# Kernel tuning notes

Hardware: AMD Instinct MI355X
Metric: run time of the kernel (lower is better)

Reference implementation:

```python
import jax, jax.numpy as jnp
import numpy as np

H = 16  # num_heads


def setup_inputs() -> dict:
    key = jax.random.key(0)
    ks = jax.random.split(key, 8)
    B, S, d, L = 1, 2048, 1024, 8
    hd = d // H
    s = 0.02
    return {
        "x": jax.random.normal(ks[0], (B, S, d), jnp.float32),
        "past_values": jax.random.normal(ks[1], (L, B, H, S, hd), jnp.float32),
        "Wqkv": jax.random.normal(ks[2], (3 * d, d), jnp.float32) * s,
        "bqkv": jax.random.normal(ks[3], (3 * d,), jnp.float32) * s,
        "Wcol": jax.random.normal(ks[4], (d, d), jnp.float32) * s,
        "bcol": jax.random.normal(ks[5], (d,), jnp.float32) * s,
        "Wout": jax.random.normal(ks[6], (d, d), jnp.float32) * s,
        "bout": jax.random.normal(ks[7], (d,), jnp.float32) * s,
    }


def reference(x, past_values, Wqkv, bqkv, Wcol, bcol, Wout, bout):
    B, S, d = x.shape
    L = past_values.shape[0]
    hd = d // H
    scale = 1.0 / np.sqrt(hd).astype(np.float32)

    qkv = x @ Wqkv.T + bqkv                       # [B,S,3d]
    q, k, v = jnp.split(qkv, 3, axis=-1)

    def heads(t):                                  # [B,S,d] -> [B,H,S,hd]
        return t.reshape(B, S, H, hd).transpose(0, 2, 1, 3)

    q_row, k, v = heads(q), heads(k), heads(v)
    q_col = heads(x @ Wcol.T + bcol)

    # causal token scores [B,H,S,S]
    token_scores = jnp.einsum('bhqd,bhkd->bhqk', q_row, k) * scale
    causal = jnp.triu(jnp.ones((S, S), bool), 1)
    token_scores = jnp.where(causal, -jnp.inf, token_scores)

    # stack past values: torch stack(dim=3) -> [B,H,S,L,hd]; permute -> [B,S,L,H*hd]
    pv = past_values.transpose(1, 3, 0, 2, 4).reshape(B, S, L, d)
    ri = pv.reshape(B, S * L, d)
    mu = ri.mean(-1, keepdims=True)
    var = ri.var(-1, keepdims=True)
    ri = (ri - mu) / jnp.sqrt(var + 1e-5)          # F.layer_norm, no affine

    Wk, bk = Wqkv[d:2 * d], bqkv[d:2 * d]
    Wv, bv = Wqkv[2 * d:], bqkv[2 * d:]
    rk = (ri @ Wk.T + bk).reshape(B, S * L, H, hd).transpose(0, 2, 1, 3).reshape(B, H, S, L, hd)
    rv = (ri @ Wv.T + bv).reshape(B, S * L, H, hd).transpose(0, 2, 1, 3).reshape(B, H, S, L, hd)

    mem_scores = jnp.einsum('bhsd,bhsld->bhsl', q_col, rk) * scale  # [B,H,S,L]

    scores = jnp.concatenate([token_scores, mem_scores], axis=-1)   # [B,H,S,S+L]
    w = jax.nn.softmax(scores, axis=-1)
    tw, mw = w[..., :S], w[..., S:]

    ctx = jnp.einsum('bhqk,bhkd->bhqd', tw, v) + jnp.einsum('bhsl,bhsld->bhsd', mw, rv)
    out = ctx.transpose(0, 2, 1, 3).reshape(B, S, d)
    return out @ Wout.T + bout
```

## Files before the change

kernel.cpp:

```cpp
#include <hip/hip_runtime.h>
#include <math.h>

#define D   1024
#define H   16
#define HD  64
#define SEQ 2048
#define LL  8
#define SCALE 0.125f

typedef __attribute__((ext_vector_type(8))) __bf16 bf16x8;
typedef __attribute__((ext_vector_type(4))) float floatx4;
typedef __attribute__((ext_vector_type(8))) unsigned short ushort8;

__device__ inline unsigned short f32_to_bf16(float f) {
    unsigned int u = __builtin_bit_cast(unsigned int, f);
    u += 0x7FFF + ((u >> 16) & 1);
    return (unsigned short)(u >> 16);
}
__device__ inline float bf2f(unsigned short u) {
    unsigned int x = (unsigned int)u << 16;
    return __builtin_bit_cast(float, x);
}
__device__ inline void load_lds16(const void* g, void* l) {
    __builtin_amdgcn_global_load_lds(
        (__attribute__((address_space(1))) void*)g,
        (__attribute__((address_space(3))) void*)l, 16, 0, 0);
}

__device__ inline void xcd_swizzle(int& bx, int& by) {
    const int gx   = gridDim.x;
    const int lin  = blockIdx.y * gx + blockIdx.x;
    const int nblk = gx * gridDim.y;
    const int virt = (lin & 7) * (nblk >> 3) + (lin >> 3);
    bx = virt % gx;
    by = virt / gx;
}

#define NQ_X    524288
#define NQ_WQKV 786432
#define NQ_WC   262144
#define NQ_WO   262144
#define LN_BLK  16384
#define CVT_BLK 7168
#define PREP_GRID (LN_BLK + CVT_BLK + 4)

__global__ __launch_bounds__(256) void prep_kernel(
    const float* __restrict__ pv, const float* __restrict__ x,
    const float* __restrict__ Wqkv, const float* __restrict__ Wcol,
    const float* __restrict__ Wout, const float* __restrict__ bqkv,
    const float* __restrict__ bcol,
    unsigned short* __restrict__ ri, unsigned short* __restrict__ xb,
    unsigned short* __restrict__ W4b, unsigned short* __restrict__ Woutb,
    float* __restrict__ b4)
{
    const int b = blockIdx.x;
    const int t = threadIdx.x;
    if (b < LN_BLK) {
        const int r = b;
        const int s = r >> 3, l = r & 7;
        const int h = t >> 4, e = (t & 15) * 4;
        const size_t src = (size_t)l * (H * SEQ * HD) + (size_t)h * (SEQ * HD)
                         + (size_t)s * HD + e;
        float4 v = *(const float4*)(pv + src);
        float sum = v.x + v.y + v.z + v.w;
        float sq  = v.x * v.x + v.y * v.y + v.z * v.z + v.w * v.w;
#pragma unroll
        for (int off = 32; off; off >>= 1) {
            sum += __shfl_xor(sum, off);
            sq  += __shfl_xor(sq, off);
        }
        __shared__ float red[8];
        if ((t & 63) == 0) { red[(t >> 6) * 2] = sum; red[(t >> 6) * 2 + 1] = sq; }
        __syncthreads();
        sum = red[0] + red[2] + red[4] + red[6];
        sq  = red[1] + red[3] + red[5] + red[7];
        const float mean = sum * (1.f / 1024.f);
        const float var  = sq * (1.f / 1024.f) - mean * mean;
        const float rstd = rsqrtf(var + 1e-5f);
        ushort4 o;
        o.x = f32_to_bf16((v.x - mean) * rstd);
        o.y = f32_to_bf16((v.y - mean) * rstd);
        o.z = f32_to_bf16((v.z - mean) * rstd);
        o.w = f32_to_bf16((v.w - mean) * rstd);
        *(ushort4*)(ri + (size_t)r * D + t * 4) = o;
    } else if (b < LN_BLK + CVT_BLK) {
        const int i = (b - LN_BLK) * 256 + t;
        const float* src; unsigned short* dst; int off;
        if (i < NQ_X)                        { src = x;    dst = xb;    off = i; }
        else if (i < NQ_X + NQ_WQKV)         { src = Wqkv; dst = W4b;   off = i - NQ_X; }
        else if (i < NQ_X + NQ_WQKV + NQ_WC) {
            float4 v = ((const float4*)Wcol)[i - NQ_X - NQ_WQKV];
            ushort4 o;
            o.x = f32_to_bf16(v.x); o.y = f32_to_bf16(v.y);
            o.z = f32_to_bf16(v.z); o.w = f32_to_bf16(v.w);
            ((ushort4*)(W4b))[NQ_WQKV + (i - NQ_X - NQ_WQKV)] = o;
            return;
        }
        else                                 { src = Wout; dst = Woutb; off = i - NQ_X - NQ_WQKV - NQ_WC; }
        float4 v = ((const float4*)src)[off];
        ushort4 o;
        o.x = f32_to_bf16(v.x); o.y = f32_to_bf16(v.y);
        o.z = f32_to_bf16(v.z); o.w = f32_to_bf16(v.w);
        ((ushort4*)dst)[off] = o;
    } else {
        const int q = (b - LN_BLK - CVT_BLK) * 256 + t;
        float4 v = (q < 768) ? ((const float4*)bqkv)[q] : ((const float4*)bcol)[q - 768];
        ((float4*)b4)[q] = v;
    }
}

__global__ __launch_bounds__(256) void wkt_kernel(
    const float* __restrict__ Wqkv, unsigned short* __restrict__ WkT)
{
    const int h = blockIdx.x >> 4, ct = blockIdx.x & 15;
    const int c0 = ct * 64;
    const int t = threadIdx.x;
    __shared__ float tile[64][68];
    {
        const int e  = t >> 2;
        const int c4 = (t & 3) * 16;
        const float* src = Wqkv + (size_t)(D + h * HD + e) * D + c0 + c4;
#pragma unroll
        for (int j = 0; j < 4; j++) {
            float4 v = ((const float4*)src)[j];
            *(float4*)&tile[e][c4 + j * 4] = v;
        }
    }
    __syncthreads();
    {
        const int c  = t >> 2;
        const int e0 = (t & 3) * 16;
        ushort8 o0, o1;
#pragma unroll
        for (int j = 0; j < 8; j++) o0[j] = f32_to_bf16(tile[e0 + j][c]);
#pragma unroll
        for (int j = 0; j < 8; j++) o1[j] = f32_to_bf16(tile[e0 + 8 + j][c]);
        unsigned short* dst = WkT + (size_t)h * (D * HD) + (size_t)(c0 + c) * HD + e0;
        *(ushort8*)dst       = o0;
        *(ushort8*)(dst + 8) = o1;
    }
}

__global__ __launch_bounds__(256) void vtr_kernel(
    const unsigned short* __restrict__ qkv4, unsigned short* __restrict__ VT)
{
    const int h = blockIdx.x & 15, kt = blockIdx.x >> 4;
    const int t = threadIdx.x;
    __shared__ unsigned short Vt[64][264];
    const int pr = t & 31, eg = t >> 5;
#pragma unroll
    for (int sub = 0; sub < 4; sub++) {
        const int j0 = kt * 256 + sub * 64;
        const unsigned short* v0 = qkv4 + (size_t)(j0 + 2 * pr) * 4096 + 2 * D + h * HD + eg * 8;
        ushort8 va = *(const ushort8*)v0;
        ushort8 vb = *(const ushort8*)(v0 + 4096);
#pragma unroll
        for (int j = 0; j < 8; j++) {
            unsigned int pk = (unsigned int)va[j] | ((unsigned int)vb[j] << 16);
            *(unsigned int*)&Vt[eg * 8 + j][sub * 64 + 2 * pr] = pk;
        }
    }
    __syncthreads();
#pragma unroll
    for (int it = 0; it < 8; it++) {
        const int idx = it * 256 + t;
        const int e = idx >> 5, ch = idx & 31;
        ushort8 v = *(const ushort8*)&Vt[e][ch * 8];
        *(ushort8*)(VT + (size_t)h * (HD * SEQ) + (size_t)e * SEQ + kt * 256 + ch * 8) = v;
    }
}

template <typename CT, bool HAS_BIAS>
__global__ __launch_bounds__(256) void gemm_bf16_kernel(
    const unsigned short* __restrict__ A, const unsigned short* __restrict__ W,
    const float* __restrict__ bias, CT* __restrict__ C,
    int K, int N, int lda, int ldw, int ldc,
    size_t zsA, size_t zsW, size_t zsC)
{
    A += (size_t)blockIdx.z * zsA;
    W += (size_t)blockIdx.z * zsW;
    C += (size_t)blockIdx.z * zsC;

    __shared__ unsigned short As[128 * 32];
    __shared__ unsigned short Ws[128 * 32];
    const int t    = threadIdx.x;
    const int wave = t >> 6, lane = t & 63;
    const int wm   = wave >> 1, wn = wave & 1;
    int bx, by;
    xcd_swizzle(bx, by);
    const int m0 = by * 128, n0 = bx * 128;

    floatx4 acc[4][4];
#pragma unroll
    for (int i = 0; i < 4; i++)
#pragma unroll
        for (int j = 0; j < 4; j++) acc[i][j] = (floatx4)0.f;

    const int lrow = lane >> 2;
    const int lcol = (lane & 3) * 8;
    const unsigned short* Ag = A + (size_t)(m0 + wave * 32 + lrow) * lda + lcol;
    const unsigned short* Wg = W + (size_t)(n0 + wave * 32 + lrow) * ldw + lcol;
    unsigned short* Asw = &As[wave * 32 * 32];
    unsigned short* Wsw = &Ws[wave * 32 * 32];
    const size_t rowskipA = (size_t)16 * lda;
    const size_t rowskipW = (size_t)16 * ldw;

    const int arow  = lane & 15;
    const int aquad = (lane >> 4) * 8;

    for (int k0 = 0; k0 < K; k0 += 32) {
        load_lds16(Ag + k0,             Asw);
        load_lds16(Ag + k0 + rowskipA,  Asw + 16 * 32);
        load_lds16(Wg + k0,             Wsw);
        load_lds16(Wg + k0 + rowskipW,  Wsw + 16 * 32);
        __syncthreads();

        bf16x8 af[4], wf[4];
#pragma unroll
        for (int mi = 0; mi < 4; mi++)
            af[mi] = *(const bf16x8*)&As[(wm * 64 + mi * 16 + arow) * 32 + aquad];
#pragma unroll
        for (int ni = 0; ni < 4; ni++)
            wf[ni] = *(const bf16x8*)&Ws[(wn * 64 + ni * 16 + arow) * 32 + aquad];
#pragma unroll
        for (int mi = 0; mi < 4; mi++)
#pragma unroll
            for (int ni = 0; ni < 4; ni++)
                acc[mi][ni] = __builtin_amdgcn_mfma_f32_16x16x32_bf16(
                    af[mi], wf[ni], acc[mi][ni], 0, 0, 0);
        __syncthreads();
    }

    const int crow = (lane >> 4) * 4, ccol = lane & 15;
#pragma unroll
    for (int mi = 0; mi < 4; mi++) {
#pragma unroll
        for (int ni = 0; ni < 4; ni++) {
            const int gm = m0 + wm * 64 + mi * 16 + crow;
            const int gn = n0 + wn * 64 + ni * 16 + ccol;
            float bb = 0.f;
            if constexpr (HAS_BIAS) bb = bias[gn];
#pragma unroll
            for (int r = 0; r < 4; r++) {
                float v = acc[mi][ni][r] + bb;
                if constexpr (sizeof(CT) == 2)
                    C[(size_t)(gm + r) * ldc + gn] = (CT)f32_to_bf16(v);
                else
                    C[(size_t)(gm + r) * ldc + gn] = v;
            }
        }
    }
}

#define US_STRIDE 1032

__global__ __launch_bounds__(256) void memsc_kernel(
    const unsigned short* __restrict__ U, const unsigned short* __restrict__ ri,
    const unsigned short* __restrict__ qkv4, const float* __restrict__ bqkv,
    float* __restrict__ scores)
{
    const int s = blockIdx.x;
    const int t = threadIdx.x;
    const int w = t >> 6, lane = t & 63;
    const int lrow = lane & 15;
    const int lkq  = (lane >> 4) * 8;

    __shared__ unsigned short Us[16 * US_STRIDE];
    __shared__ union {
        unsigned short riS[8 * US_STRIDE];
        float red[4][16][16];
    } R;
    __shared__ float qbS[H];

    {
        const unsigned short* src = U + (size_t)s * (H * D);
#pragma unroll
        for (int j = 0; j < 8; j++) {
            const int c = j * 256 + t;
            const int row = c >> 7, col = (c & 127) * 8;
            *(ushort8*)&Us[row * US_STRIDE + col] =
                *(const ushort8*)(src + row * D + col);
        }
    }
    {
        const unsigned short* src = ri + (size_t)s * (LL * D);
#pragma unroll
        for (int j = 0; j < 4; j++) {
            const int c = j * 256 + t;
            const int row = c >> 7, col = (c & 127) * 8;
            *(ushort8*)&R.riS[row * US_STRIDE + col] =
                *(const ushort8*)(src + row * D + col);
        }
    }
    {
        const int h = t >> 4, sub = t & 15;
        const unsigned short* qc = qkv4 + (size_t)s * 4096 + 3 * D + h * HD + sub * 4;
        const float* bk = bqkv + D + h * HD + sub * 4;
        float acc = 0.f;
#pragma unroll
        for (int j = 0; j < 4; j++) acc += bf2f(qc[j]) * bk[j];
#pragma unroll
        for (int off = 1; off < 16; off <<= 1) acc += __shfl_xor(acc, off);
        if (sub == 0) qbS[h] = acc;
    }
    __syncthreads();

    floatx4 acc = (floatx4)0.f;
    const int kbase = w * 256;
#pragma unroll
    for (int step = 0; step < 8; step++) {
        const int k0 = kbase + step * 32;
        bf16x8 af = *(const bf16x8*)&Us[lrow * US_STRIDE + k0 + lkq];
        bf16x8 bf = {};
        if (lrow < 8) bf = *(const bf16x8*)&R.riS[lrow * US_STRIDE + k0 + lkq];
        acc = __builtin_amdgcn_mfma_f32_16x16x32_bf16(af, bf, acc, 0, 0, 0);
    }
    __syncthreads();

    {
        const int crow = (lane >> 4) * 4, ccol = lane & 15;
#pragma unroll
        for (int r = 0; r < 4; r++) R.red[w][crow + r][ccol] = acc[r];
    }
    __syncthreads();

    if (t < H * LL) {
        const int h = t >> 3, l = t & 7;
        float v = R.red[0][h][l] + R.red[1][h][l] + R.red[2][h][l] + R.red[3][h][l];
        scores[((size_t)s * H + h) * LL + l] = (v + qbS[h]) * SCALE;
    }
}

__global__ __launch_bounds__(256, 3) void attn_split_kernel(
    const unsigned short* __restrict__ qkv4, const unsigned short* __restrict__ VT,
    float* __restrict__ Opart, float2* __restrict__ mlpart)
{
    const int t    = threadIdx.x;
    const int w    = t >> 6, lane = t & 63;
    const int lrow = lane & 15;
    const int lk   = (lane >> 4) * 8;
    const int rrow = (lane >> 4) * 4;
    const int lin  = blockIdx.x;
    const int hsp  = lin & 63, g = lin >> 6;
    const int s    = hsp >> 4, h = hsp & 15;
    const int qt   = 31 - g;
    const int q0   = qt * 64;
    const int n    = qt + 1;
    const int lo   = (s * n) >> 2, hi = ((s + 1) * n) >> 2;
    const int part = (h * 32 + qt) * 4 + s;

    __shared__ unsigned short Ks[2][64 * 72];
    __shared__ unsigned short Vs[2][64 * 72];
    __shared__ unsigned short Pb[4][16 * 72];
    unsigned short* Pw = Pb[w];

    bf16x8 qreg[2];
#pragma unroll
    for (int kst = 0; kst < 2; kst++) {
        ushort8 qu = *(const ushort8*)(qkv4 + (size_t)(q0 + w * 16 + lrow) * 4096
                                       + h * HD + kst * 32 + lk);
        ushort8 qs;
#pragma unroll
        for (int j = 0; j < 8; j++) qs[j] = f32_to_bf16(bf2f(qu[j]) * SCALE);
        qreg[kst] = __builtin_bit_cast(bf16x8, qs);
    }

    const int srow = t >> 3;
    const int scol = (t & 7) * 8;
    const unsigned short* Kg = qkv4 + D + h * HD;
    const unsigned short* Vg = VT + (size_t)h * (HD * SEQ);

    bf16x8 kr0, kr1, vr0, vr1;
    float m_i[4], l_i[4];
    floatx4 Oacc[4];
#pragma unroll
    for (int r = 0; r < 4; r++) { m_i[r] = -1e30f; l_i[r] = 0.f; }
#pragma unroll
    for (int et = 0; et < 4; et++) Oacc[et] = (floatx4)0.f;

    if (lo < hi) {
        const int j0 = lo * 64;
        kr0 = *(const bf16x8*)(Kg + (size_t)(j0 + srow) * 4096 + scol);
        kr1 = *(const bf16x8*)(Kg + (size_t)(j0 + 32 + srow) * 4096 + scol);
        vr0 = *(const bf16x8*)(Vg + (size_t)srow * SEQ + j0 + scol);
        vr1 = *(const bf16x8*)(Vg + (size_t)(srow + 32) * SEQ + j0 + scol);
    }

    int cur = 0;
    for (int jt = lo; jt < hi; jt++) {
        const int j0 = jt * 64;
        *(bf16x8*)&Ks[cur][srow * 72 + scol]        = kr0;
        *(bf16x8*)&Ks[cur][(srow + 32) * 72 + scol] = kr1;
        *(bf16x8*)&Vs[cur][srow * 72 + scol]        = vr0;
        *(bf16x8*)&Vs[cur][(srow + 32) * 72 + scol] = vr1;
        if (jt + 1 < hi) {
            const int j0n = (jt + 1) * 64;
            kr0 = *(const bf16x8*)(Kg + (size_t)(j0n + srow) * 4096 + scol);
            kr1 = *(const bf16x8*)(Kg + (size_t)(j0n + 32 + srow) * 4096 + scol);
            vr0 = *(const bf16x8*)(Vg + (size_t)srow * SEQ + j0n + scol);
            vr1 = *(const bf16x8*)(Vg + (size_t)(srow + 32) * SEQ + j0n + scol);
        }
        __syncthreads();

        floatx4 S[4];
#pragma unroll
        for (int nt = 0; nt < 4; nt++) S[nt] = (floatx4)0.f;
        __builtin_amdgcn_s_setprio(1);
#pragma unroll
        for (int kst = 0; kst < 2; kst++) {
#pragma unroll
            for (int nt = 0; nt < 4; nt++) {
                bf16x8 bk = *(const bf16x8*)&Ks[cur][(nt * 16 + lrow) * 72 + kst * 32 + lk];
                S[nt] = __builtin_amdgcn_mfma_f32_16x16x32_bf16(qreg[kst], bk, S[nt], 0, 0, 0);
            }
        }
        __builtin_amdgcn_s_setprio(0);

        if (jt != qt) {
#pragma unroll
            for (int r = 0; r < 4; r++) {
                float sc[4];
#pragma unroll
                for (int nt = 0; nt < 4; nt++) sc[nt] = S[nt][r];
                float mx = fmaxf(fmaxf(sc[0], sc[1]), fmaxf(sc[2], sc[3]));
#pragma unroll
                for (int off = 1; off < 16; off <<= 1)
                    mx = fmaxf(mx, __shfl_xor(mx, off));
                const bool keep = __all(mx <= m_i[r] + 8.f);
                const float newm = keep ? m_i[r] : fmaxf(m_i[r], mx);
                float ps = 0.f;
#pragma unroll
                for (int nt = 0; nt < 4; nt++) {
                    float pe = __expf(sc[nt] - newm);
                    ps += pe;
                    Pw[(rrow + r) * 72 + nt * 16 + lrow] = f32_to_bf16(pe);
                }
#pragma unroll
                for (int off = 1; off < 16; off <<= 1)
                    ps += __shfl_xor(ps, off);
                if (keep) {
                    l_i[r] += ps;
                } else {
                    const float alpha = __expf(m_i[r] - newm);
                    m_i[r] = newm;
                    l_i[r] = l_i[r] * alpha + ps;
#pragma unroll
                    for (int et = 0; et < 4; et++) Oacc[et][r] *= alpha;
                }
            }
        } else {
#pragma unroll
            for (int r = 0; r < 4; r++) {
                const int qg = q0 + w * 16 + rrow + r;
                float sc[4];
                float mx = -1e30f;
#pragma unroll
                for (int nt = 0; nt < 4; nt++) {
                    sc[nt] = S[nt][r];
                    if (j0 + nt * 16 + lrow > qg) sc[nt] = -1e30f;
                    mx = fmaxf(mx, sc[nt]);
                }
#pragma unroll
                for (int off = 1; off < 16; off <<= 1)
                    mx = fmaxf(mx, __shfl_xor(mx, off));
                const float newm  = fmaxf(m_i[r], mx);
                const float alpha = __expf(m_i[r] - newm);
                m_i[r] = newm;
                float ps = 0.f;
#pragma unroll
                for (int nt = 0; nt < 4; nt++) {
                    float pe = __expf(sc[nt] - newm);
                    ps += pe;
                    Pw[(rrow + r) * 72 + nt * 16 + lrow] = f32_to_bf16(pe);
                }
#pragma unroll
                for (int off = 1; off < 16; off <<= 1)
                    ps += __shfl_xor(ps, off);
                l_i[r] = l_i[r] * alpha + ps;
#pragma unroll
                for (int et = 0; et < 4; et++) Oacc[et][r] *= alpha;
            }
        }

        __builtin_amdgcn_s_setprio(1);
#pragma unroll
        for (int kst = 0; kst < 2; kst++) {
            bf16x8 ap = *(const bf16x8*)&Pw[lrow * 72 + kst * 32 + lk];
#pragma unroll
            for (int et = 0; et < 4; et++) {
                bf16x8 bv = *(const bf16x8*)&Vs[cur][(et * 16 + lrow) * 72 + kst * 32 + lk];
                Oacc[et] = __builtin_amdgcn_mfma_f32_16x16x32_bf16(ap, bv, Oacc[et], 0, 0, 0);
            }
        }
        __builtin_amdgcn_s_setprio(0);
        cur ^= 1;
    }

#pragma unroll
    for (int r = 0; r < 4; r++) {
        const int ql = w * 16 + rrow + r;
        if (lrow == 0) mlpart[(size_t)part * 64 + ql] = make_float2(m_i[r], l_i[r]);
#pragma unroll
        for (int et = 0; et < 4; et++)
            Opart[((size_t)part * 64 + ql) * 64 + et * 16 + lrow] = Oacc[et][r];
    }
}

__global__ __launch_bounds__(256) void attn_merge_kernel(
    const float* __restrict__ Opart, const float2* __restrict__ mlpart,
    const float* __restrict__ scores,
    float* __restrict__ tok, float* __restrict__ mwf, float* __restrict__ Pmem)
{
    const int blk = blockIdx.x;
    const int h = blk >> 5, qt = blk & 31;
    const int q0 = qt * 64;
    const int t = threadIdx.x, tx = t & 15, ty = t >> 4;
    const size_t pb = (size_t)blk * 4;
#pragma unroll
    for (int i = 0; i < 4; i++) {
        const int qi = ty * 4 + i, qg = q0 + qi;
        float2 ml[4];
#pragma unroll
        for (int ps = 0; ps < 4; ps++) ml[ps] = mlpart[(pb + ps) * 64 + qi];
        const float* msp = scores + ((size_t)qg * H + h) * LL;
        float ms[LL];
#pragma unroll
        for (int l = 0; l < LL; l++) ms[l] = msp[l];
        float M = ml[0].x;
#pragma unroll
        for (int ps = 1; ps < 4; ps++) M = fmaxf(M, ml[ps].x);
#pragma unroll
        for (int l = 0; l < LL; l++) M = fmaxf(M, ms[l]);
        float f[4], L = 0.f;
#pragma unroll
        for (int ps = 0; ps < 4; ps++) { f[ps] = __expf(ml[ps].x - M); L += ml[ps].y * f[ps]; }
        float pm[LL];
#pragma unroll
        for (int l = 0; l < LL; l++) { pm[l] = __expf(ms[l] - M); L += pm[l]; }
        const float rl = 1.f / L;
        float4 o = make_float4(0.f, 0.f, 0.f, 0.f);
#pragma unroll
        for (int ps = 0; ps < 4; ps++) {
            const float fs = f[ps] * rl;
            float4 op = *(const float4*)&Opart[((pb + ps) * 64 + qi) * 64 + tx * 4];
            o.x += op.x * fs; o.y += op.y * fs; o.z += op.z * fs; o.w += op.w * fs;
        }
        *(float4*)&tok[(size_t)qg * D + h * HD + tx * 4] = o;
        if (tx == 0) {
            float* mw = mwf + ((size_t)qg * H + h) * LL;
            float psum = 0.f;
#pragma unroll
            for (int l = 0; l < LL; l++) { float v = pm[l] * rl; mw[l] = v; psum += v; }
            Pmem[(size_t)qg * H + h] = psum;
        }
    }
}

__global__ __launch_bounds__(256) void rbar_kernel(
    const float* __restrict__ mwf, const unsigned short* __restrict__ ri,
    unsigned short* __restrict__ rbar)
{
    const int s = blockIdx.x, t = threadIdx.x;
    __shared__ unsigned short riS[LL * D];
    __shared__ float wS[H * LL];
    {
        const unsigned short* src = ri + (size_t)s * (LL * D);
#pragma unroll
        for (int j = 0; j < 4; j++) {
            const int off = (j * 256 + t) * 8;
            *(ushort8*)&riS[off] = *(const ushort8*)(src + off);
        }
    }
    if (t < H * LL) wS[t] = mwf[(size_t)s * (H * LL) + t];
    __syncthreads();
    const int c4 = t * 4;
#pragma unroll
    for (int hh = 0; hh < H; hh++) {
        float v0 = 0.f, v1 = 0.f, v2 = 0.f, v3 = 0.f;
#pragma unroll
        for (int l = 0; l < LL; l++) {
            const float wv = wS[hh * LL + l];
            ushort4 rr = *(const ushort4*)&riS[l * D + c4];
            v0 += wv * bf2f(rr.x); v1 += wv * bf2f(rr.y);
            v2 += wv * bf2f(rr.z); v3 += wv * bf2f(rr.w);
        }
        ushort4 o;
        o.x = f32_to_bf16(v0); o.y = f32_to_bf16(v1);
        o.z = f32_to_bf16(v2); o.w = f32_to_bf16(v3);
        *(ushort4*)(rbar + ((size_t)hh * SEQ + s) * D + c4) = o;
    }
}

__global__ __launch_bounds__(256) void gemm_ctx_kernel(
    const unsigned short* __restrict__ rbar, const unsigned short* __restrict__ W4,
    const float* __restrict__ bqkv, const float* __restrict__ Pmem,
    const float* __restrict__ tok, unsigned short* __restrict__ ctx)
{
    const int mt = blockIdx.x;
    const int h  = blockIdx.y;
    const unsigned short* A  = rbar + (size_t)h * SEQ * D + (size_t)mt * 128 * D;
    const unsigned short* Wv = W4 + (size_t)(2 * D + h * HD) * D;
    const float* bv = bqkv + 2 * D + h * HD;

    __shared__ unsigned short As[128 * 32];
    __shared__ unsigned short Ws[64 * 32];
    const int t    = threadIdx.x;
    const int wave = t >> 6, lane = t & 63;

    floatx4 acc[2][4];
#pragma unroll
    for (int i = 0; i < 2; i++)
#pragma unroll
        for (int j = 0; j < 4; j++) acc[i][j] = (floatx4)0.f;

    const int lrow = lane >> 2;
    const int lcol = (lane & 3) * 8;
    const unsigned short* Ag = A  + (size_t)(wave * 32 + lrow) * D + lcol;
    const unsigned short* Wg = Wv + (size_t)(wave * 32 + lrow) * D + lcol;
    unsigned short* Asw = &As[wave * 32 * 32];
    unsigned short* Wsw = &Ws[wave * 32 * 32];
    const size_t rowskip = (size_t)16 * D;

    const int arow  = lane & 15;
    const int aquad = (lane >> 4) * 8;

    for (int k0 = 0; k0 < D; k0 += 32) {
        load_lds16(Ag + k0,           Asw);
        load_lds16(Ag + k0 + rowskip, Asw + 16 * 32);
        if (wave < 2) {
            load_lds16(Wg + k0,           Wsw);
            load_lds16(Wg + k0 + rowskip, Wsw + 16 * 32);
        }
        __syncthreads();

        bf16x8 af[2], wf[4];
#pragma unroll
        for (int mi = 0; mi < 2; mi++)
            af[mi] = *(const bf16x8*)&As[(wave * 32 + mi * 16 + arow) * 32 + aquad];
#pragma unroll
        for (int ni = 0; ni < 4; ni++)
            wf[ni] = *(const bf16x8*)&Ws[(ni * 16 + arow) * 32 + aquad];
#pragma unroll
        for (int mi = 0; mi < 2; mi++)
#pragma unroll
            for (int ni = 0; ni < 4; ni++)
                acc[mi][ni] = __builtin_amdgcn_mfma_f32_16x16x32_bf16(
                    af[mi], wf[ni], acc[mi][ni], 0, 0, 0);
        __syncthreads();
    }

    const int crow = (lane >> 4) * 4, ccol = lane & 15;
#pragma unroll
    for (int mi = 0; mi < 2; mi++) {
#pragma unroll
        for (int ni = 0; ni < 4; ni++) {
            const int e  = ni * 16 + ccol;
            const float bb = bv[e];
#pragma unroll
            for (int r = 0; r < 4; r++) {
                const int grow = mt * 128 + wave * 32 + mi * 16 + crow + r;
                float v = acc[mi][ni][r] + bb * Pmem[(size_t)grow * H + h]
                          + tok[(size_t)grow * D + h * HD + e];
                ctx[(size_t)grow * D + h * HD + e] = f32_to_bf16(v);
            }
        }
    }
}

extern "C" void kernel_launch(void* const* d_in, const int* in_sizes, int n_in,
                              void* d_out, int out_size, void* d_ws, size_t ws_size,
                              hipStream_t stream)
{
    const float* x    = (const float*)d_in[0];
    const float* pv   = (const float*)d_in[1];
    const float* Wqkv = (const float*)d_in[2];
    const float* bqkv = (const float*)d_in[3];
    const float* Wcol = (const float*)d_in[4];
    const float* bcol = (const float*)d_in[5];
    const float* Wout = (const float*)d_in[6];
    const float* bout = (const float*)d_in[7];
    float* out = (float*)d_out;

    char* p = (char*)d_ws;
    unsigned short* x_bf    = (unsigned short*)p; p += (size_t)2048 * 1024 * 2;
    unsigned short* W4_bf   = (unsigned short*)p; p += (size_t)4096 * 1024 * 2;
    unsigned short* Wout_bf = (unsigned short*)p; p += (size_t)1024 * 1024 * 2;
    float*          b4      = (float*)p;          p += (size_t)4096 * 4;
    unsigned short* ri_bf   = (unsigned short*)p; p += (size_t)16384 * 1024 * 2;
    unsigned short* qkv4_bf = (unsigned short*)p; p += (size_t)2048 * 4096 * 2;
    unsigned short* WkT_bf  = (unsigned short*)p; p += (size_t)16 * 1024 * 64 * 2;
    unsigned short* VT_bf   = (unsigned short*)p; p += (size_t)16 * 64 * 2048 * 2;
    float*          scores  = (float*)p;          p += (size_t)2048 * 16 * 8 * 4;
    float*          mwf     = (float*)p;          p += (size_t)2048 * 16 * 8 * 4;
    float*          Pmem    = (float*)p;          p += (size_t)2048 * 16 * 4;
    float*          tok     = (float*)p;          p += (size_t)2048 * 1024 * 4;
    unsigned short* ctx_bf  = (unsigned short*)p; p += (size_t)2048 * 1024 * 2;
    float*          Opart   = (float*)p;          p += (size_t)2048 * 64 * 64 * 4;
    float2*         mlpart  = (float2*)p;         p += (size_t)2048 * 64 * 8;
    unsigned short* Urb     = (unsigned short*)p; p += (size_t)16 * 2048 * 1024 * 2;

    prep_kernel<<<PREP_GRID, 256, 0, stream>>>(pv, x, Wqkv, Wcol, Wout, bqkv, bcol,
                                               ri_bf, x_bf, W4_bf, Wout_bf, b4);
    wkt_kernel<<<256, 256, 0, stream>>>(Wqkv, WkT_bf);
    gemm_bf16_kernel<unsigned short, true><<<dim3(32, 16, 1), 256, 0, stream>>>(
        x_bf, W4_bf, b4, qkv4_bf, 1024, 4096, 1024, 1024, 4096, 0, 0, 0);
    vtr_kernel<<<128, 256, 0, stream>>>(qkv4_bf, VT_bf);
    gemm_bf16_kernel<unsigned short, false><<<dim3(8, 16, 16), 256, 0, stream>>>(
        qkv4_bf + 3 * D, WkT_bf, nullptr, Urb, 64, 1024, 4096, 64, H * D,
        (size_t)HD, (size_t)D * HD, (size_t)D);
    memsc_kernel<<<2048, 256, 0, stream>>>(Urb, ri_bf, qkv4_bf, bqkv, scores);
    attn_split_kernel<<<2048, 256, 0, stream>>>(qkv4_bf, VT_bf, Opart, mlpart);
    attn_merge_kernel<<<512, 256, 0, stream>>>(Opart, mlpart, scores, tok, mwf, Pmem);
    rbar_kernel<<<2048, 256, 0, stream>>>(mwf, ri_bf, Urb);
    gemm_ctx_kernel<<<dim3(16, 16), 256, 0, stream>>>(Urb, W4_bf, bqkv, Pmem, tok, ctx_bf);
    gemm_bf16_kernel<float, true><<<dim3(8, 16, 1), 256, 0, stream>>>(
        ctx_bf, Wout_bf, bout, out, 1024, 1024, 1024, 1024, 1024, 0, 0, 0);
}
```

Measured before the change: 319.4 us.

## Transpose attention MFMAs to keep P in registers and drop LDS round-trip

Swaps the MFMA operand order so each lane holds one query row's scores, which makes the softmax max/sum reductions per-lane plus two cross-lane shuffles. The probability tile is packed to bf16 with a hardware pack instruction and rearranged with lane shuffles into the A-operand layout, so the per-wave LDS P buffer and its stores and loads go away. Output partials are written as float4, and launch bounds are raised to allow four blocks per CU. The cost is a more intricate shuffle/select sequence and extra register pressure at the higher occupancy target.

```diff
diff --git a/kernel.cpp b/kernel.cpp
--- a/kernel.cpp
+++ b/kernel.cpp
@@ -11,6 +11,7 @@
 typedef __attribute__((ext_vector_type(8))) __bf16 bf16x8;
 typedef __attribute__((ext_vector_type(4))) float floatx4;
 typedef __attribute__((ext_vector_type(8))) unsigned short ushort8;
+typedef __attribute__((ext_vector_type(4))) unsigned int uintx4;
 
 __device__ inline unsigned short f32_to_bf16(float f) {
     unsigned int u = __builtin_bit_cast(unsigned int, f);
@@ -20,6 +21,11 @@
 __device__ inline float bf2f(unsigned short u) {
     unsigned int x = (unsigned int)u << 16;
     return __builtin_bit_cast(float, x);
+}
+__device__ inline unsigned int cvt_pk_bf16(float lo, float hi) {
+    unsigned int r;
+    asm("v_cvt_pk_bf16_f32 %0, %1, %2" : "=v"(r) : "v"(lo), "v"(hi));
+    return r;
 }
 __device__ inline void load_lds16(const void* g, void* l) {
     __builtin_amdgcn_global_load_lds(
@@ -331,7 +337,7 @@
     }
 }
 
-__global__ __launch_bounds__(256, 3) void attn_split_kernel(
+__global__ __launch_bounds__(256, 4) void attn_split_kernel(
     const unsigned short* __restrict__ qkv4, const unsigned short* __restrict__ VT,
     float* __restrict__ Opart, float2* __restrict__ mlpart)
 {
@@ -339,7 +345,8 @@
     const int w    = t >> 6, lane = t & 63;
     const int lrow = lane & 15;
     const int lk   = (lane >> 4) * 8;
-    const int rrow = (lane >> 4) * 4;
+    const int qd   = lane >> 4;
+    const int hi2  = qd >> 1, lo2 = qd & 1;
     const int lin  = blockIdx.x;
     const int hsp  = lin & 63, g = lin >> 6;
     const int s    = hsp >> 4, h = hsp & 15;
@@ -351,8 +358,6 @@
 
     __shared__ unsigned short Ks[2][64 * 72];
     __shared__ unsigned short Vs[2][64 * 72];
-    __shared__ unsigned short Pb[4][16 * 72];
-    unsigned short* Pw = Pb[w];
 
     bf16x8 qreg[2];
 #pragma unroll
@@ -364,6 +369,7 @@
         for (int j = 0; j < 8; j++) qs[j] = f32_to_bf16(bf2f(qu[j]) * SCALE);
         qreg[kst] = __builtin_bit_cast(bf16x8, qs);
     }
+    const int qg = q0 + w * 16 + lrow;
 
     const int srow = t >> 3;
     const int scol = (t & 7) * 8;
@@ -371,10 +377,8 @@
     const unsigned short* Vg = VT + (size_t)h * (HD * SEQ);
 
     bf16x8 kr0, kr1, vr0, vr1;
-    float m_i[4], l_i[4];
+    float m_i = -1e30f, l_i = 0.f;
     floatx4 Oacc[4];
-#pragma unroll
-    for (int r = 0; r < 4; r++) { m_i[r] = -1e30f; l_i[r] = 0.f; }
 #pragma unroll
     for (int et = 0; et < 4; et++) Oacc[et] = (floatx4)0.f;
 
@@ -411,99 +415,101 @@
 #pragma unroll
             for (int nt = 0; nt < 4; nt++) {
                 bf16x8 bk = *(const bf16x8*)&Ks[cur][(nt * 16 + lrow) * 72 + kst * 32 + lk];
-                S[nt] = __builtin_amdgcn_mfma_f32_16x16x32_bf16(qreg[kst], bk, S[nt], 0, 0, 0);
+                S[nt] = __builtin_amdgcn_mfma_f32_16x16x32_bf16(bk, qreg[kst], S[nt], 0, 0, 0);
             }
         }
         __builtin_amdgcn_s_setprio(0);
 
-        if (jt != qt) {
-#pragma unroll
-            for (int r = 0; r < 4; r++) {
-                float sc[4];
-#pragma unroll
-                for (int nt = 0; nt < 4; nt++) sc[nt] = S[nt][r];
-                float mx = fmaxf(fmaxf(sc[0], sc[1]), fmaxf(sc[2], sc[3]));
-#pragma unroll
-                for (int off = 1; off < 16; off <<= 1)
-                    mx = fmaxf(mx, __shfl_xor(mx, off));
-                const bool keep = __all(mx <= m_i[r] + 8.f);
-                const float newm = keep ? m_i[r] : fmaxf(m_i[r], mx);
-                float ps = 0.f;
-#pragma unroll
-                for (int nt = 0; nt < 4; nt++) {
-                    float pe = __expf(sc[nt] - newm);
-                    ps += pe;
-                    Pw[(rrow + r) * 72 + nt * 16 + lrow] = f32_to_bf16(pe);
-                }
-#pragma unroll
-                for (int off = 1; off < 16; off <<= 1)
-                    ps += __shfl_xor(ps, off);
-                if (keep) {
-                    l_i[r] += ps;
-                } else {
-                    const float alpha = __expf(m_i[r] - newm);
-                    m_i[r] = newm;
-                    l_i[r] = l_i[r] * alpha + ps;
-#pragma unroll
-                    for (int et = 0; et < 4; et++) Oacc[et][r] *= alpha;
-                }
-            }
-        } else {
-#pragma unroll
-            for (int r = 0; r < 4; r++) {
-                const int qg = q0 + w * 16 + rrow + r;
-                float sc[4];
-                float mx = -1e30f;
-#pragma unroll
-                for (int nt = 0; nt < 4; nt++) {
-                    sc[nt] = S[nt][r];
-                    if (j0 + nt * 16 + lrow > qg) sc[nt] = -1e30f;
-                    mx = fmaxf(mx, sc[nt]);
-                }
-#pragma unroll
-                for (int off = 1; off < 16; off <<= 1)
-                    mx = fmaxf(mx, __shfl_xor(mx, off));
-                const float newm  = fmaxf(m_i[r], mx);
-                const float alpha = __expf(m_i[r] - newm);
-                m_i[r] = newm;
-                float ps = 0.f;
-#pragma unroll
-                for (int nt = 0; nt < 4; nt++) {
-                    float pe = __expf(sc[nt] - newm);
-                    ps += pe;
-                    Pw[(rrow + r) * 72 + nt * 16 + lrow] = f32_to_bf16(pe);
-                }
-#pragma unroll
-                for (int off = 1; off < 16; off <<= 1)
-                    ps += __shfl_xor(ps, off);
-                l_i[r] = l_i[r] * alpha + ps;
-#pragma unroll
-                for (int et = 0; et < 4; et++) Oacc[et][r] *= alpha;
-            }
-        }
+        const bool diag = (jt == qt);
+        if (diag) {
+#pragma unroll
+            for (int nt = 0; nt < 4; nt++)
+#pragma unroll
+                for (int r = 0; r < 4; r++)
+                    if (j0 + nt * 16 + qd * 4 + r > qg) S[nt][r] = -1e30f;
+        }
+        float mx = -1e30f;
+#pragma unroll
+        for (int nt = 0; nt < 4; nt++)
+            mx = fmaxf(mx, fmaxf(fmaxf(S[nt][0], S[nt][1]), fmaxf(S[nt][2], S[nt][3])));
+        mx = fmaxf(mx, __shfl_xor(mx, 16));
+        mx = fmaxf(mx, __shfl_xor(mx, 32));
+        const bool keep = !diag && __all(mx <= m_i + 8.f);
+        if (!keep) {
+            const float newm = fmaxf(m_i, mx);
+            const float a = __expf(m_i - newm);
+            m_i = newm;
+            l_i *= a;
+#pragma unroll
+            for (int et = 0; et < 4; et++) Oacc[et] *= a;
+        }
+
+        float ps = 0.f;
+        unsigned int up[4][2];
+#pragma unroll
+        for (int nt = 0; nt < 4; nt++) {
+            float p0 = __expf(S[nt][0] - m_i);
+            float p1 = __expf(S[nt][1] - m_i);
+            float p2 = __expf(S[nt][2] - m_i);
+            float p3 = __expf(S[nt][3] - m_i);
+            ps += (p0 + p1) + (p2 + p3);
+            up[nt][0] = cvt_pk_bf16(p0, p1);
+            up[nt][1] = cvt_pk_bf16(p2, p3);
+        }
+        ps += __shfl_xor(ps, 16);
+        ps += __shfl_xor(ps, 32);
+        l_i += ps;
+
+        unsigned int s0 = hi2 ? up[0][0] : up[1][0];
+        unsigned int s1 = hi2 ? up[0][1] : up[1][1];
+        unsigned int s2 = hi2 ? up[2][0] : up[3][0];
+        unsigned int s3 = hi2 ? up[2][1] : up[3][1];
+        s0 = __shfl_xor(s0, 32); s1 = __shfl_xor(s1, 32);
+        s2 = __shfl_xor(s2, 32); s3 = __shfl_xor(s3, 32);
+        const unsigned int ownA0 = hi2 ? up[1][0] : up[0][0];
+        const unsigned int ownA1 = hi2 ? up[1][1] : up[0][1];
+        const unsigned int ownB0 = hi2 ? up[3][0] : up[2][0];
+        const unsigned int ownB1 = hi2 ? up[3][1] : up[2][1];
+        const bool keepOwn = (hi2 == lo2);
+        unsigned int eA0 = keepOwn ? s0 : ownA0;
+        unsigned int eA1 = keepOwn ? s1 : ownA1;
+        unsigned int eB0 = keepOwn ? s2 : ownB0;
+        unsigned int eB1 = keepOwn ? s3 : ownB1;
+        eA0 = __shfl_xor(eA0, 16); eA1 = __shfl_xor(eA1, 16);
+        eB0 = __shfl_xor(eB0, 16); eB1 = __shfl_xor(eB1, 16);
+        const unsigned int kA0 = keepOwn ? ownA0 : s0;
+        const unsigned int kA1 = keepOwn ? ownA1 : s1;
+        const unsigned int kB0 = keepOwn ? ownB0 : s2;
+        const unsigned int kB1 = keepOwn ? ownB1 : s3;
+        uintx4 fA = { lo2 ? eA0 : kA0, lo2 ? eA1 : kA1,
+                      lo2 ? kA0 : eA0, lo2 ? kA1 : eA1 };
+        uintx4 fB = { lo2 ? eB0 : kB0, lo2 ? eB1 : kB1,
+                      lo2 ? kB0 : eB0, lo2 ? kB1 : eB1 };
+        bf16x8 apA = __builtin_bit_cast(bf16x8, fA);
+        bf16x8 apB = __builtin_bit_cast(bf16x8, fB);
 
         __builtin_amdgcn_s_setprio(1);
 #pragma unroll
-        for (int kst = 0; kst < 2; kst++) {
-            bf16x8 ap = *(const bf16x8*)&Pw[lrow * 72 + kst * 32 + lk];
-#pragma unroll
-            for (int et = 0; et < 4; et++) {
-                bf16x8 bv = *(const bf16x8*)&Vs[cur][(et * 16 + lrow) * 72 + kst * 32 + lk];
-                Oacc[et] = __builtin_amdgcn_mfma_f32_16x16x32_bf16(ap, bv, Oacc[et], 0, 0, 0);
-            }
+        for (int et = 0; et < 4; et++) {
+            bf16x8 bv = *(const bf16x8*)&Vs[cur][(et * 16 + lrow) * 72 + lk];
+            Oacc[et] = __builtin_amdgcn_mfma_f32_16x16x32_bf16(bv, apA, Oacc[et], 0, 0, 0);
+        }
+#pragma unroll
+        for (int et = 0; et < 4; et++) {
+            bf16x8 bv = *(const bf16x8*)&Vs[cur][(et * 16 + lrow) * 72 + 32 + lk];
+            Oacc[et] = __builtin_amdgcn_mfma_f32_16x16x32_bf16(bv, apB, Oacc[et], 0, 0, 0);
         }
         __builtin_amdgcn_s_setprio(0);
         cur ^= 1;
     }
 
 #pragma unroll
-    for (int r = 0; r < 4; r++) {
-        const int ql = w * 16 + rrow + r;
-        if (lrow == 0) mlpart[(size_t)part * 64 + ql] = make_float2(m_i[r], l_i[r]);
-#pragma unroll
-        for (int et = 0; et < 4; et++)
-            Opart[((size_t)part * 64 + ql) * 64 + et * 16 + lrow] = Oacc[et][r];
-    }
+    for (int et = 0; et < 4; et++) {
+        float4 o = make_float4(Oacc[et][0], Oacc[et][1], Oacc[et][2], Oacc[et][3]);
+        *(float4*)&Opart[((size_t)part * 64 + w * 16 + lrow) * 64 + et * 16 + qd * 4] = o;
+    }
+    if (qd == 0)
+        mlpart[(size_t)part * 64 + w * 16 + lrow] = make_float2(m_i, l_i);
 }
 
 __global__ __launch_bounds__(256) void attn_merge_kernel(
```

New measurement: 304.7 us. 1.05x faster.
